# Kernel optimization log

Hardware: AMD Instinct MI355X
Metric: run time of the kernel (lower is better)

The kernel has to match this reference:

```python
import jax, jax.numpy as jnp
import numpy as np

EPS = 1e-6  # flax LayerNorm default

def _layer_norm(x, scale, bias):
    mu = jnp.mean(x, axis=-1, keepdims=True)
    var = jnp.mean(jnp.square(x - mu), axis=-1, keepdims=True)
    return (x - mu) * jax.lax.rsqrt(var + EPS) * scale + bias

def setup_inputs() -> dict:
    key = jax.random.key(0)
    ks = jax.random.split(key, 8)
    B, S, D_in, D_h, D_out, N = 4, 2048, 1024, 2048, 1024, 6
    init = lambda k, shape, fan_in: jax.random.normal(k, shape, jnp.float32) / np.sqrt(fan_in)
    return {
        "x": jax.random.normal(ks[0], (B, S, D_in), jnp.float32),
        "ln1_scale": jnp.ones((D_in,), jnp.float32),
        "ln1_bias": jnp.zeros((D_in,), jnp.float32),
        "w1": init(ks[1], (D_in, D_h), D_in),
        "b1": jnp.zeros((D_h,), jnp.float32),
        "block_ln_scales": jnp.ones((N, D_h), jnp.float32),
        "block_ln_biases": jnp.zeros((N, D_h), jnp.float32),
        "block_ws": init(ks[2], (N, D_h, D_h), D_h),
        "block_bs": jnp.zeros((N, D_h), jnp.float32),
        "ln2_scale": jnp.ones((D_h,), jnp.float32),
        "ln2_bias": jnp.zeros((D_h,), jnp.float32),
        "w2": init(ks[3], (D_h, D_out), D_h),
        "b2": jnp.zeros((D_out,), jnp.float32),
    }

def reference(x, ln1_scale, ln1_bias, w1, b1, block_ln_scales, block_ln_biases,
              block_ws, block_bs, ln2_scale, ln2_bias, w2, b2):
    # stem: LN -> Linear -> SiLU
    h = _layer_norm(x, ln1_scale, ln1_bias)
    h = jax.nn.silu(jnp.einsum('bsd,dh->bsh', h, w1) + b1)

    # residual blocks via scan over stacked params
    def block(h, params):
        s, b, w, lb = params
        y = _layer_norm(h, s, b)
        y = jax.nn.silu(jnp.einsum('bsh,hk->bsk', y, w) + lb)
        return h + y, None

    h, _ = jax.lax.scan(block, h, (block_ln_scales, block_ln_biases, block_ws, block_bs))

    # head: LN -> Linear
    h = _layer_norm(h, ln2_scale, ln2_bias)
    return jnp.einsum('bsh,ho->bso', h, w2) + b2
```

## Files before the change

kernel.cpp:

```cpp
#include <hip/hip_runtime.h>
#include <hip/hip_bf16.h>

typedef short short8 __attribute__((ext_vector_type(8)));
typedef float f32x4 __attribute__((ext_vector_type(4)));

#define AS1(p) ((const __attribute__((address_space(1))) void*)(p))
#define AS3(p) ((__attribute__((address_space(3))) void*)(p))

__device__ __forceinline__ ushort f2bf(float f) {
  __hip_bfloat16 h = __float2bfloat16(f);
  return *reinterpret_cast<const ushort*>(&h);
}
__device__ __forceinline__ float bfu2f(ushort u) {
  unsigned int x = ((unsigned int)u) << 16;
  float f;
  __builtin_memcpy(&f, &x, 4);
  return f;
}
__device__ __forceinline__ float silu_f(float v) { return v / (1.f + __expf(-v)); }

template<int NV>
__global__ __launch_bounds__(256) void ln_bf16_k(
    const float* __restrict__ in, const float* __restrict__ sc,
    const float* __restrict__ bi, ushort* __restrict__ out)
{
  const int D = NV * 1024;
  const long row = blockIdx.x;
  const int tx = threadIdx.x;
  const float* p = in + row * (long)D;
  float4 v[NV];
  float s = 0.f, s2 = 0.f;
#pragma unroll
  for (int t = 0; t < NV; ++t) {
    v[t] = *reinterpret_cast<const float4*>(p + t * 1024 + tx * 4);
    s  += v[t].x + v[t].y + v[t].z + v[t].w;
    s2 += v[t].x * v[t].x + v[t].y * v[t].y + v[t].z * v[t].z + v[t].w * v[t].w;
  }
#pragma unroll
  for (int o = 1; o < 64; o <<= 1) { s += __shfl_xor(s, o); s2 += __shfl_xor(s2, o); }
  __shared__ float red[2][4];
  const int wave = tx >> 6;
  if ((tx & 63) == 0) { red[0][wave] = s; red[1][wave] = s2; }
  __syncthreads();
  s  = red[0][0] + red[0][1] + red[0][2] + red[0][3];
  s2 = red[1][0] + red[1][1] + red[1][2] + red[1][3];
  const float mu   = s / D;
  const float rstd = rsqrtf(s2 / D - mu * mu + 1e-6f);
#pragma unroll
  for (int t = 0; t < NV; ++t) {
    const int d = t * 1024 + tx * 4;
    float4 g = *reinterpret_cast<const float4*>(sc + d);
    float4 b = *reinterpret_cast<const float4*>(bi + d);
    ushort4 o;
    o.x = f2bf((v[t].x - mu) * rstd * g.x + b.x);
    o.y = f2bf((v[t].y - mu) * rstd * g.y + b.y);
    o.z = f2bf((v[t].z - mu) * rstd * g.z + b.z);
    o.w = f2bf((v[t].w - mu) * rstd * g.w + b.w);
    *reinterpret_cast<ushort4*>(out + row * (long)D + d) = o;
  }
}

__global__ __launch_bounds__(256) void ln_stats_k(
    const ushort* __restrict__ in, float2* __restrict__ stats)
{
  const long row = blockIdx.x;
  const int tx = threadIdx.x;
  short8 v8 = *reinterpret_cast<const short8*>(in + row * 2048 + tx * 8);
  float s = 0.f, s2 = 0.f;
#pragma unroll
  for (int j = 0; j < 8; ++j) {
    const float v = bfu2f((ushort)v8[j]);
    s += v; s2 += v * v;
  }
#pragma unroll
  for (int o = 1; o < 64; o <<= 1) { s += __shfl_xor(s, o); s2 += __shfl_xor(s2, o); }
  __shared__ float red[2][4];
  const int wave = tx >> 6;
  if ((tx & 63) == 0) { red[0][wave] = s; red[1][wave] = s2; }
  __syncthreads();
  if (tx == 0) {
    s  = red[0][0] + red[0][1] + red[0][2] + red[0][3];
    s2 = red[1][0] + red[1][1] + red[1][2] + red[1][3];
    const float mu   = s * (1.f / 2048.f);
    const float rstd = rsqrtf(s2 * (1.f / 2048.f) - mu * mu + 1e-6f);
    stats[row] = make_float2(mu * rstd, rstd);
  }
}

__global__ __launch_bounds__(256) void transpose_bf16_k(
    const float* __restrict__ in, ushort* __restrict__ out, int K, int N)
{
  __shared__ float tile[64][65];
  const int k0 = blockIdx.y * 64, n0 = blockIdx.x * 64;
  const int tx = threadIdx.x, ty = threadIdx.y;
#pragma unroll
  for (int r = ty; r < 64; r += 4)
    tile[r][tx] = in[(long)(k0 + r) * N + n0 + tx];
  __syncthreads();
#pragma unroll
  for (int r = ty; r < 64; r += 4)
    out[(long)(n0 + r) * K + k0 + tx] = f2bf(tile[tx][r]);
}

__global__ __launch_bounds__(256) void transpose_scale_k(
    const float* __restrict__ in0, const float* __restrict__ g0,
    const float* __restrict__ beta0, ushort* __restrict__ out0,
    float2* __restrict__ uvw0, int K, int N)
{
  __shared__ float tile[64][65];
  const int z = blockIdx.z;
  const float* in    = in0 + (long)z * K * N;
  const float* g     = g0 + (long)z * K;
  const float* beta  = beta0 + (long)z * K;
  ushort* out        = out0 + (long)z * K * N;
  float2* uvw        = uvw0 + (long)z * N;
  const int k0 = blockIdx.y * 64, n0 = blockIdx.x * 64;
  const int tx = threadIdx.x, ty = threadIdx.y;
  float pu = 0.f, pv = 0.f;
#pragma unroll
  for (int r = ty; r < 64; r += 4) {
    const float w  = in[(long)(k0 + r) * N + n0 + tx];
    const float ws = g[k0 + r] * w;
    tile[r][tx] = ws;
    pu += ws;
    pv += beta[k0 + r] * w;
  }
  atomicAdd(&uvw[n0 + tx].x, pu);
  atomicAdd(&uvw[n0 + tx].y, pv);
  __syncthreads();
#pragma unroll
  for (int r = ty; r < 64; r += 4)
    out[(long)(n0 + r) * K + k0 + tx] = f2bf(tile[tx][r]);
}

__global__ __launch_bounds__(512) void combine_k(
    float* __restrict__ out, const float* __restrict__ part)
{
  const long i = ((long)blockIdx.x * 512 + threadIdx.x) * 4;
  float4 a = *reinterpret_cast<const float4*>(out + i);
  float4 b = *reinterpret_cast<const float4*>(part + i);
  a.x += b.x; a.y += b.y; a.z += b.z; a.w += b.w;
  *reinterpret_cast<float4*>(out + i) = a;
}

#define STG(gsrc, ldst)                                                          \
  __builtin_amdgcn_global_load_lds(AS1(gsrc),          AS3(ldst),          16, 0, 0); \
  __builtin_amdgcn_global_load_lds(AS1((gsrc) + offQ), AS3((ldst) + 8192), 16, 0, 0)

#define ldsA(B, H) (ldsW + (B) * 65536 + (H) * 16384)
#define ldsB(B, H) (ldsW + (B) * 65536 + 32768 + (H) * 16384)

#define RD_AF(DST, DB, MH, KS)                                                  \
  _Pragma("unroll") for (int i_ = 0; i_ < 4; ++i_)                              \
    DST[i_] = *(const short8*)(smem + (DB) * 65536 + aOff + ((MH) * 4 + i_) * 2048 + rdk[(KS)])

#define RD_BF(DST, DB, KS)                                                      \
  _Pragma("unroll") for (int j_ = 0; j_ < 4; ++j_)                              \
    DST[j_] = *(const short8*)(smem + (DB) * 65536 + bOff + j_ * 2048 + rdk[(KS)])

#define MFMA16(AREG, MH, BREG)                                                  \
  _Pragma("unroll") for (int i_ = 0; i_ < 4; ++i_)                              \
  _Pragma("unroll") for (int j_ = 0; j_ < 4; ++j_)                              \
    acc[(MH) * 4 + i_][j_] = __builtin_amdgcn_mfma_f32_16x16x32_bf16(           \
        AREG[i_], BREG[j_], acc[(MH) * 4 + i_][j_], 0, 0, 0)

#define BARRIER __builtin_amdgcn_s_barrier()
#define SP1 __builtin_amdgcn_s_setprio(1)
#define SP0 __builtin_amdgcn_s_setprio(0)
#define SBAR __builtin_amdgcn_sched_barrier(0)
#define LGKMW(N) do { asm volatile("s_waitcnt lgkmcnt(" #N ")"); SBAR; } while (0)
#define W4 do { asm volatile("s_waitcnt vmcnt(4)" ::: "memory"); SBAR; } while (0)
#define W0 do { asm volatile("s_waitcnt vmcnt(0)" ::: "memory"); SBAR; } while (0)
#define WN do {} while (0)

#define DO_TILE(DB, S1, AO, S2, BO, WAITE)                                      \
  RD_AF(afx, DB, 0, 0);                                                         \
  RD_BF(bf, DB, 0);                                                             \
  RD_AF(afy, DB, 1, 0);                                                         \
  if (S1) { STG(aP + (AO), ldsA((DB) ^ 1, 0));                                  \
            STG(aP + (AO) + offH, ldsA((DB) ^ 1, 1)); }                         \
  LGKMW(4);                                                                     \
  SP1; MFMA16(afx, 0, bf); SP0;                                                 \
  RD_AF(afx, DB, 0, 1);                                                         \
  LGKMW(4);                                                                     \
  SP1; MFMA16(afy, 1, bf); SP0;                                                 \
  RD_BF(bf, DB, 1);                                                             \
  SBAR;                                                                         \
  RD_AF(afy, DB, 1, 1);                                                         \
  LGKMW(4);                                                                     \
  SP1; MFMA16(afx, 0, bf); SP0;                                                 \
  BARRIER;                                                                      \
  if (S2) { STG(bP + (BO), ldsB(DB, 0));                                        \
            STG(bP + (BO) + offH, ldsB(DB, 1)); }                               \
  LGKMW(0);                                                                     \
  SP1; MFMA16(afy, 1, bf); SP0;                                                 \
  WAITE;                                                                        \
  BARRIER;

template<int MODE>
__global__ __launch_bounds__(512, 2) void gemm256_k(
    const ushort* __restrict__ A, const ushort* __restrict__ Bt,
    const float* __restrict__ bias, const float2* __restrict__ stats,
    const float2* __restrict__ uvw, const ushort* __restrict__ Rin,
    void* __restrict__ Cv, float* __restrict__ Cv2,
    int M, int N, int K, int ld)
{
  extern __shared__ char smem[];
  const int tid = threadIdx.x;
  const int lane = tid & 63, wid = tid >> 6;
  const int wr = wid >> 2, wc = wid & 3;
  const int nbx = N >> 8;

  int bid;
  {
    const int b = blockIdx.x;
    const int cpx = gridDim.x >> 3;
    bid = (b & 7) * cpx + (b >> 3);
  }
  int kb = 0;
  if (MODE == 5) { kb = bid >> 7; bid &= 127; }
  const int bx = bid % nbx, by = bid / nbx;
  const long m0 = (long)by << 8, n0 = (long)bx << 8;

  const int srow = tid >> 3;
  const int scol = (((tid & 7) * 16) ^ (((tid >> 3) & 7) << 4)) >> 1;
  const ushort* aP = A  + (long)kb * 1024 + (m0 + srow) * (long)ld + scol;
  const ushort* bP = Bt + (long)kb * 1024 + (n0 + srow) * (long)ld + scol;
  const long offH = 128L * ld, offQ = 64L * ld;
  char* ldsW = smem + wid * 1024;

  int rdk[2];
  rdk[0] = (((lane >> 4) * 16)     ) ^ ((lane & 7) << 4);
  rdk[1] = (((lane >> 4) * 16) + 64) ^ ((lane & 7) << 4);
  const int aOff = wr * 16384 + (lane & 15) * 128;
  const int bOff = 32768 + (wc >> 1) * 16384 + ((wc & 1) * 64 + (lane & 15)) * 128;

  f32x4 acc[8][4] = {};
  const int NT = K >> 6;

  STG(aP,      ldsA(0, 0));  STG(aP + offH,      ldsA(0, 1));
  STG(bP,      ldsB(0, 0));  STG(bP + offH,      ldsB(0, 1));
  STG(bP + 64, ldsB(1, 0));  STG(bP + 64 + offH, ldsB(1, 1));
  W4;
  BARRIER;

  short8 afx[4], afy[4], bf[4];
  for (int t = 0; t < NT - 2; t += 2) {
    DO_TILE(0, 1,  64, 1, 128, W4)
    DO_TILE(1, 1, 128, 1, 192, W4)
    aP += 128; bP += 128;
  }
  DO_TILE(0, 1, 64, 0, 0, W0)
  DO_TILE(1, 0,  0, 0, 0, WN)

  if (MODE == 0) {
#pragma unroll
    for (int j = 0; j < 4; ++j) {
      const long col = n0 + wc * 64 + j * 16 + (lane & 15);
      const float bj = bias[col];
#pragma unroll
      for (int i = 0; i < 8; ++i) {
        const long rowb = m0 + wr * 128 + i * 16 + ((lane >> 4) << 2);
#pragma unroll
        for (int r = 0; r < 4; ++r) {
          const float v = acc[i][j][r] + bj;
          ((ushort*)Cv)[(rowb + r) * N + col] = f2bf(silu_f(v));
        }
      }
    }
  } else {
    float2 uvv[4];
    float  bj4[4];
    long   col4[4];
#pragma unroll
    for (int j = 0; j < 4; ++j) {
      col4[j] = n0 + wc * 64 + j * 16 + (lane & 15);
      uvv[j]  = uvw[col4[j]];
      bj4[j]  = bias[col4[j]];
    }
    float* dst = (MODE == 5 && kb == 1) ? Cv2 : (float*)Cv;
    const float cw = (MODE == 5 && kb == 1) ? 0.f : 1.f;
#pragma unroll
    for (int i = 0; i < 8; ++i) {
      const long rowb = m0 + wr * 128 + i * 16 + ((lane >> 4) << 2);
#pragma unroll
      for (int r = 0; r < 4; ++r) {
        const long row = rowb + r;
        const float2 ms = stats[row];
#pragma unroll
        for (int j = 0; j < 4; ++j) {
          const long idx = row * (long)N + col4[j];
          if (MODE == 3) {
            const float v = ms.y * acc[i][j][r] - ms.x * uvv[j].x + uvv[j].y + bj4[j];
            ((ushort*)Cv)[idx] = f2bf(bfu2f(Rin[idx]) + silu_f(v));
          } else {
            const float v = ms.y * acc[i][j][r]
                          + cw * (uvv[j].y + bj4[j] - ms.x * uvv[j].x);
            dst[idx] = v;
          }
        }
      }
    }
  }
}

extern "C" void kernel_launch(void* const* d_in, const int* in_sizes, int n_in,
                              void* d_out, int out_size, void* d_ws, size_t ws_size,
                              hipStream_t stream) {
  const float* x     = (const float*)d_in[0];
  const float* ln1_s = (const float*)d_in[1];
  const float* ln1_b = (const float*)d_in[2];
  const float* w1    = (const float*)d_in[3];
  const float* b1    = (const float*)d_in[4];
  const float* bln_s = (const float*)d_in[5];
  const float* bln_b = (const float*)d_in[6];
  const float* bws   = (const float*)d_in[7];
  const float* bbs   = (const float*)d_in[8];
  const float* ln2_s = (const float*)d_in[9];
  const float* ln2_b = (const float*)d_in[10];
  const float* w2    = (const float*)d_in[11];
  const float* b2    = (const float*)d_in[12];
  float* out = (float*)d_out;

  const int M = 8192;
  char* ws = (char*)d_ws;
  ushort* h0    = (ushort*)ws;
  ushort* h1    = (ushort*)(ws + 33554432);
  ushort* Abf   = h1;
  ushort* wt    = (ushort*)(ws + 67108864);
  float2* uvw   = (float2*)(ws + 125829120);
  float2* stats = (float2*)(ws + 125829120 + 131072);
  const long W1T = 0;
  const long BLK = 2097152;
  const long W2T = BLK + 6L * 4194304;

  (void)hipFuncSetAttribute((const void*)gemm256_k<0>,
      hipFuncAttributeMaxDynamicSharedMemorySize, 131072);
  (void)hipFuncSetAttribute((const void*)gemm256_k<3>,
      hipFuncAttributeMaxDynamicSharedMemorySize, 131072);
  (void)hipFuncSetAttribute((const void*)gemm256_k<5>,
      hipFuncAttributeMaxDynamicSharedMemorySize, 131072);

  (void)hipMemsetAsync(uvw, 0, 7 * 2048 * sizeof(float2), stream);

  dim3 tb(64, 4);
  transpose_bf16_k<<<dim3(32, 16), tb, 0, stream>>>(w1, wt + W1T, 1024, 2048);
  transpose_scale_k<<<dim3(32, 32, 6), tb, 0, stream>>>(
      bws, bln_s, bln_b, wt + BLK, uvw, 2048, 2048);
  transpose_scale_k<<<dim3(16, 32, 1), tb, 0, stream>>>(
      w2, ln2_s, ln2_b, wt + W2T, uvw + 6L * 2048, 2048, 1024);

  ln_bf16_k<1><<<M, 256, 0, stream>>>(x, ln1_s, ln1_b, Abf);
  gemm256_k<0><<<32 * 8, 512, 131072, stream>>>(
      Abf, wt + W1T, b1, nullptr, nullptr, nullptr,
      (void*)h0, nullptr, M, 2048, 1024, 1024);

  ushort* hin = h0;
  ushort* hout = h1;
  for (int i = 0; i < 6; ++i) {
    ln_stats_k<<<M, 256, 0, stream>>>(hin, stats);
    gemm256_k<3><<<32 * 8, 512, 131072, stream>>>(
        hin, wt + BLK + (long)i * 4194304, bbs + i * 2048, stats,
        uvw + (long)i * 2048, hin, (void*)hout, nullptr, M, 2048, 2048, 2048);
    ushort* tmp = hin; hin = hout; hout = tmp;
  }

  float* part = (float*)h1;
  ln_stats_k<<<M, 256, 0, stream>>>(hin, stats);
  gemm256_k<5><<<32 * 4 * 2, 512, 131072, stream>>>(
      hin, wt + W2T, b2, stats, uvw + 6L * 2048, nullptr,
      (void*)out, part, M, 1024, 1024, 2048);
  combine_k<<<4096, 512, 0, stream>>>(out, part);
}
```

Before: 650.4 us.

## Fuse LayerNorm row statistics into GEMM epilogue with partial-sum reduction

Result: slower. 688.2 us (+5.8%).

```diff
diff --git a/kernel.cpp b/kernel.cpp
--- a/kernel.cpp
+++ b/kernel.cpp
@@ -60,33 +60,6 @@
   }
 }
 
-__global__ __launch_bounds__(256) void ln_stats_k(
-    const ushort* __restrict__ in, float2* __restrict__ stats)
-{
-  const long row = blockIdx.x;
-  const int tx = threadIdx.x;
-  short8 v8 = *reinterpret_cast<const short8*>(in + row * 2048 + tx * 8);
-  float s = 0.f, s2 = 0.f;
-#pragma unroll
-  for (int j = 0; j < 8; ++j) {
-    const float v = bfu2f((ushort)v8[j]);
-    s += v; s2 += v * v;
-  }
-#pragma unroll
-  for (int o = 1; o < 64; o <<= 1) { s += __shfl_xor(s, o); s2 += __shfl_xor(s2, o); }
-  __shared__ float red[2][4];
-  const int wave = tx >> 6;
-  if ((tx & 63) == 0) { red[0][wave] = s; red[1][wave] = s2; }
-  __syncthreads();
-  if (tx == 0) {
-    s  = red[0][0] + red[0][1] + red[0][2] + red[0][3];
-    s2 = red[1][0] + red[1][1] + red[1][2] + red[1][3];
-    const float mu   = s * (1.f / 2048.f);
-    const float rstd = rsqrtf(s2 * (1.f / 2048.f) - mu * mu + 1e-6f);
-    stats[row] = make_float2(mu * rstd, rstd);
-  }
-}
-
 __global__ __launch_bounds__(256) void transpose_bf16_k(
     const float* __restrict__ in, ushort* __restrict__ out, int K, int N)
 {
@@ -131,6 +104,22 @@
 #pragma unroll
   for (int r = ty; r < 64; r += 4)
     out[(long)(n0 + r) * K + k0 + tx] = f2bf(tile[tx][r]);
+}
+
+__global__ __launch_bounds__(256) void stats_reduce_k(
+    const float2* __restrict__ pstat, float2* __restrict__ stats)
+{
+  const int row = blockIdx.x * 256 + threadIdx.x;
+  const float4* p = reinterpret_cast<const float4*>(pstat + (long)row * 32);
+  float s = 0.f, s2 = 0.f;
+#pragma unroll
+  for (int q = 0; q < 16; ++q) {
+    const float4 v = p[q];
+    s += v.x + v.z; s2 += v.y + v.w;
+  }
+  const float mu   = s * (1.f / 2048.f);
+  const float rstd = rsqrtf(s2 * (1.f / 2048.f) - mu * mu + 1e-6f);
+  stats[row] = make_float2(mu * rstd, rstd);
 }
 
 __global__ __launch_bounds__(512) void combine_k(
@@ -202,7 +191,7 @@
     const ushort* __restrict__ A, const ushort* __restrict__ Bt,
     const float* __restrict__ bias, const float2* __restrict__ stats,
     const float2* __restrict__ uvw, const ushort* __restrict__ Rin,
-    void* __restrict__ Cv, float* __restrict__ Cv2,
+    float2* __restrict__ pstat, void* __restrict__ Cv, float* __restrict__ Cv2,
     int M, int N, int K, int ld)
 {
   extern __shared__ char smem[];
@@ -253,52 +242,50 @@
   DO_TILE(0, 1, 64, 0, 0, W0)
   DO_TILE(1, 0,  0, 0, 0, WN)
 
-  if (MODE == 0) {
-#pragma unroll
-    for (int j = 0; j < 4; ++j) {
-      const long col = n0 + wc * 64 + j * 16 + (lane & 15);
-      const float bj = bias[col];
-#pragma unroll
-      for (int i = 0; i < 8; ++i) {
-        const long rowb = m0 + wr * 128 + i * 16 + ((lane >> 4) << 2);
-#pragma unroll
-        for (int r = 0; r < 4; ++r) {
-          const float v = acc[i][j][r] + bj;
-          ((ushort*)Cv)[(rowb + r) * N + col] = f2bf(silu_f(v));
+  long  col4[4];
+  float bj4[4];
+  float2 uvv[4];
+#pragma unroll
+  for (int j = 0; j < 4; ++j) {
+    col4[j] = n0 + wc * 64 + j * 16 + (lane & 15);
+    bj4[j]  = bias[col4[j]];
+    if (MODE != 0) uvv[j] = uvw[col4[j]];
+  }
+  float* dst = (MODE == 5 && kb == 1) ? Cv2 : (float*)Cv;
+  const float cw = (MODE == 5 && kb == 1) ? 0.f : 1.f;
+#pragma unroll
+  for (int i = 0; i < 8; ++i) {
+#pragma unroll
+    for (int r = 0; r < 4; ++r) {
+      const long row = m0 + wr * 128 + i * 16 + ((lane >> 4) << 2) + r;
+      float2 ms = make_float2(0.f, 1.f);
+      if (MODE != 0) ms = stats[row];
+      float ps = 0.f, ps2 = 0.f;
+#pragma unroll
+      for (int j = 0; j < 4; ++j) {
+        const long idx = row * (long)N + col4[j];
+        if (MODE == 0) {
+          const float hv = silu_f(acc[i][j][r] + bj4[j]);
+          ((ushort*)Cv)[idx] = f2bf(hv);
+          ps += hv; ps2 += hv * hv;
+        } else if (MODE == 3) {
+          const float v = ms.y * acc[i][j][r] - ms.x * uvv[j].x + uvv[j].y + bj4[j];
+          const float hv = bfu2f(Rin[idx]) + silu_f(v);
+          ((ushort*)Cv)[idx] = f2bf(hv);
+          ps += hv; ps2 += hv * hv;
+        } else {
+          const float v = ms.y * acc[i][j][r]
+                        + cw * (uvv[j].y + bj4[j] - ms.x * uvv[j].x);
+          dst[idx] = v;
         }
       }
-    }
-  } else {
-    float2 uvv[4];
-    float  bj4[4];
-    long   col4[4];
-#pragma unroll
-    for (int j = 0; j < 4; ++j) {
-      col4[j] = n0 + wc * 64 + j * 16 + (lane & 15);
-      uvv[j]  = uvw[col4[j]];
-      bj4[j]  = bias[col4[j]];
-    }
-    float* dst = (MODE == 5 && kb == 1) ? Cv2 : (float*)Cv;
-    const float cw = (MODE == 5 && kb == 1) ? 0.f : 1.f;
-#pragma unroll
-    for (int i = 0; i < 8; ++i) {
-      const long rowb = m0 + wr * 128 + i * 16 + ((lane >> 4) << 2);
-#pragma unroll
-      for (int r = 0; r < 4; ++r) {
-        const long row = rowb + r;
-        const float2 ms = stats[row];
-#pragma unroll
-        for (int j = 0; j < 4; ++j) {
-          const long idx = row * (long)N + col4[j];
-          if (MODE == 3) {
-            const float v = ms.y * acc[i][j][r] - ms.x * uvv[j].x + uvv[j].y + bj4[j];
-            ((ushort*)Cv)[idx] = f2bf(bfu2f(Rin[idx]) + silu_f(v));
-          } else {
-            const float v = ms.y * acc[i][j][r]
-                          + cw * (uvv[j].y + bj4[j] - ms.x * uvv[j].x);
-            dst[idx] = v;
-          }
-        }
+      if (MODE == 0 || MODE == 3) {
+        ps  += __shfl_xor(ps, 1);  ps2 += __shfl_xor(ps2, 1);
+        ps  += __shfl_xor(ps, 2);  ps2 += __shfl_xor(ps2, 2);
+        ps  += __shfl_xor(ps, 4);  ps2 += __shfl_xor(ps2, 4);
+        ps  += __shfl_xor(ps, 8);  ps2 += __shfl_xor(ps2, 8);
+        if ((lane & 15) == 0)
+          pstat[row * 32 + bx * 4 + wc] = make_float2(ps, ps2);
       }
     }
   }
@@ -330,6 +317,7 @@
   ushort* wt    = (ushort*)(ws + 67108864);
   float2* uvw   = (float2*)(ws + 125829120);
   float2* stats = (float2*)(ws + 125829120 + 131072);
+  float2* pstat = (float2*)(ws + 125829120 + 131072 + 65536);
   const long W1T = 0;
   const long BLK = 2097152;
   const long W2T = BLK + 6L * 4194304;
@@ -352,23 +340,24 @@
 
   ln_bf16_k<1><<<M, 256, 0, stream>>>(x, ln1_s, ln1_b, Abf);
   gemm256_k<0><<<32 * 8, 512, 131072, stream>>>(
-      Abf, wt + W1T, b1, nullptr, nullptr, nullptr,
+      Abf, wt + W1T, b1, nullptr, nullptr, nullptr, pstat,
       (void*)h0, nullptr, M, 2048, 1024, 1024);
+  stats_reduce_k<<<32, 256, 0, stream>>>(pstat, stats);
 
   ushort* hin = h0;
   ushort* hout = h1;
   for (int i = 0; i < 6; ++i) {
-    ln_stats_k<<<M, 256, 0, stream>>>(hin, stats);
     gemm256_k<3><<<32 * 8, 512, 131072, stream>>>(
         hin, wt + BLK + (long)i * 4194304, bbs + i * 2048, stats,
-        uvw + (long)i * 2048, hin, (void*)hout, nullptr, M, 2048, 2048, 2048);
+        uvw + (long)i * 2048, hin, pstat, (void*)hout, nullptr,
+        M, 2048, 2048, 2048);
+    stats_reduce_k<<<32, 256, 0, stream>>>(pstat, stats);
     ushort* tmp = hin; hin = hout; hout = tmp;
   }
 
   float* part = (float*)h1;
-  ln_stats_k<<<M, 256, 0, stream>>>(hin, stats);
   gemm256_k<5><<<32 * 4 * 2, 512, 131072, stream>>>(
-      hin, wt + W2T, b2, stats, uvw + 6L * 2048, nullptr,
+      hin, wt + W2T, b2, stats, uvw + 6L * 2048, nullptr, nullptr,
       (void*)out, part, M, 1024, 1024, 2048);
   combine_k<<<4096, 512, 0, stream>>>(out, part);
 }
```

## Switch GEMM to 32x32x16 MFMA tiles and replace atomic uv sums with reduction

Applied to the files above, without the earlier changes.

Measured after the change: 699.7 us. +7.6%, slower.

```diff
diff --git a/kernel.cpp b/kernel.cpp
--- a/kernel.cpp
+++ b/kernel.cpp
@@ -2,7 +2,7 @@
 #include <hip/hip_bf16.h>
 
 typedef short short8 __attribute__((ext_vector_type(8)));
-typedef float f32x4 __attribute__((ext_vector_type(4)));
+typedef float f32x16 __attribute__((ext_vector_type(16)));
 
 #define AS1(p) ((const __attribute__((address_space(1))) void*)(p))
 #define AS3(p) ((__attribute__((address_space(3))) void*)(p))
@@ -105,15 +105,15 @@
 __global__ __launch_bounds__(256) void transpose_scale_k(
     const float* __restrict__ in0, const float* __restrict__ g0,
     const float* __restrict__ beta0, ushort* __restrict__ out0,
-    float2* __restrict__ uvw0, int K, int N)
+    float2* __restrict__ pup, int K, int N)
 {
   __shared__ float tile[64][65];
+  __shared__ float2 pred[4][64];
   const int z = blockIdx.z;
   const float* in    = in0 + (long)z * K * N;
   const float* g     = g0 + (long)z * K;
   const float* beta  = beta0 + (long)z * K;
   ushort* out        = out0 + (long)z * K * N;
-  float2* uvw        = uvw0 + (long)z * N;
   const int k0 = blockIdx.y * 64, n0 = blockIdx.x * 64;
   const int tx = threadIdx.x, ty = threadIdx.y;
   float pu = 0.f, pv = 0.f;
@@ -125,12 +125,29 @@
     pu += ws;
     pv += beta[k0 + r] * w;
   }
-  atomicAdd(&uvw[n0 + tx].x, pu);
-  atomicAdd(&uvw[n0 + tx].y, pv);
+  pred[ty][tx] = make_float2(pu, pv);
   __syncthreads();
+  if (ty == 0) {
+    const float2 a = pred[0][tx], b = pred[1][tx], c = pred[2][tx], d = pred[3][tx];
+    const long ZN = (long)gridDim.z * N;
+    pup[(long)blockIdx.y * ZN + (long)z * N + n0 + tx] =
+        make_float2(a.x + b.x + c.x + d.x, a.y + b.y + c.y + d.y);
+  }
 #pragma unroll
   for (int r = ty; r < 64; r += 4)
     out[(long)(n0 + r) * K + k0 + tx] = f2bf(tile[tx][r]);
+}
+
+__global__ __launch_bounds__(256) void uv_reduce_k(
+    const float2* __restrict__ pup, float2* __restrict__ uvw, int NK, int ZN)
+{
+  const int c = blockIdx.x * 256 + threadIdx.x;
+  float sx = 0.f, sy = 0.f;
+  for (int k = 0; k < NK; ++k) {
+    const float2 v = pup[(long)k * ZN + c];
+    sx += v.x; sy += v.y;
+  }
+  uvw[c] = make_float2(sx, sy);
 }
 
 __global__ __launch_bounds__(512) void combine_k(
@@ -150,19 +167,19 @@
 #define ldsA(B, H) (ldsW + (B) * 65536 + (H) * 16384)
 #define ldsB(B, H) (ldsW + (B) * 65536 + 32768 + (H) * 16384)
 
-#define RD_AF(DST, DB, MH, KS)                                                  \
+#define RD_A32(DST, DB, KS)                                                     \
   _Pragma("unroll") for (int i_ = 0; i_ < 4; ++i_)                              \
-    DST[i_] = *(const short8*)(smem + (DB) * 65536 + aOff + ((MH) * 4 + i_) * 2048 + rdk[(KS)])
-
-#define RD_BF(DST, DB, KS)                                                      \
-  _Pragma("unroll") for (int j_ = 0; j_ < 4; ++j_)                              \
-    DST[j_] = *(const short8*)(smem + (DB) * 65536 + bOff + j_ * 2048 + rdk[(KS)])
-
-#define MFMA16(AREG, MH, BREG)                                                  \
-  _Pragma("unroll") for (int i_ = 0; i_ < 4; ++i_)                              \
-  _Pragma("unroll") for (int j_ = 0; j_ < 4; ++j_)                              \
-    acc[(MH) * 4 + i_][j_] = __builtin_amdgcn_mfma_f32_16x16x32_bf16(           \
-        AREG[i_], BREG[j_], acc[(MH) * 4 + i_][j_], 0, 0, 0)
+    DST[i_] = *(const short8*)(smem + (DB) * 65536 + aB + i_ * 4096 + rdk32[(KS)])
+
+#define RD_B32(DST, DB, KS)                                                     \
+  _Pragma("unroll") for (int j_ = 0; j_ < 2; ++j_)                              \
+    DST[j_] = *(const short8*)(smem + (DB) * 65536 + bB + j_ * 4096 + rdk32[(KS)])
+
+#define MFMA8(AR, BR)                                                           \
+  _Pragma("unroll") for (int rt_ = 0; rt_ < 4; ++rt_)                           \
+  _Pragma("unroll") for (int ct_ = 0; ct_ < 2; ++ct_)                           \
+    acc[rt_][ct_] = __builtin_amdgcn_mfma_f32_32x32x16_bf16(                    \
+        AR[rt_], BR[ct_], acc[rt_][ct_], 0, 0, 0)
 
 #define BARRIER __builtin_amdgcn_s_barrier()
 #define SP1 __builtin_amdgcn_s_setprio(1)
@@ -173,27 +190,28 @@
 #define W0 do { asm volatile("s_waitcnt vmcnt(0)" ::: "memory"); SBAR; } while (0)
 #define WN do {} while (0)
 
-#define DO_TILE(DB, S1, AO, S2, BO, WAITE)                                      \
-  RD_AF(afx, DB, 0, 0);                                                         \
-  RD_BF(bf, DB, 0);                                                             \
-  RD_AF(afy, DB, 1, 0);                                                         \
+#define DO_TILE32(DB, S1, AO, S2, BO, WAITE)                                    \
+  RD_A32(ax, DB, 0);                                                            \
+  RD_B32(bx, DB, 0);                                                            \
   if (S1) { STG(aP + (AO), ldsA((DB) ^ 1, 0));                                  \
             STG(aP + (AO) + offH, ldsA((DB) ^ 1, 1)); }                         \
-  LGKMW(4);                                                                     \
-  SP1; MFMA16(afx, 0, bf); SP0;                                                 \
-  RD_AF(afx, DB, 0, 1);                                                         \
-  LGKMW(4);                                                                     \
-  SP1; MFMA16(afy, 1, bf); SP0;                                                 \
-  RD_BF(bf, DB, 1);                                                             \
-  SBAR;                                                                         \
-  RD_AF(afy, DB, 1, 1);                                                         \
-  LGKMW(4);                                                                     \
-  SP1; MFMA16(afx, 0, bf); SP0;                                                 \
+  RD_A32(ay, DB, 1);                                                            \
+  RD_B32(by, DB, 1);                                                            \
+  LGKMW(6);                                                                     \
+  SP1; MFMA8(ax, bx); SP0;                                                      \
+  RD_A32(ax, DB, 2);                                                            \
+  RD_B32(bx, DB, 2);                                                            \
+  LGKMW(6);                                                                     \
+  SP1; MFMA8(ay, by); SP0;                                                      \
+  RD_A32(ay, DB, 3);                                                            \
+  RD_B32(by, DB, 3);                                                            \
+  LGKMW(6);                                                                     \
+  SP1; MFMA8(ax, bx); SP0;                                                      \
   BARRIER;                                                                      \
   if (S2) { STG(bP + (BO), ldsB(DB, 0));                                        \
             STG(bP + (BO) + offH, ldsB(DB, 1)); }                               \
   LGKMW(0);                                                                     \
-  SP1; MFMA16(afy, 1, bf); SP0;                                                 \
+  SP1; MFMA8(ay, by); SP0;                                                      \
   WAITE;                                                                        \
   BARRIER;
 
@@ -229,13 +247,14 @@
   const long offH = 128L * ld, offQ = 64L * ld;
   char* ldsW = smem + wid * 1024;
 
-  int rdk[2];
-  rdk[0] = (((lane >> 4) * 16)     ) ^ ((lane & 7) << 4);
-  rdk[1] = (((lane >> 4) * 16) + 64) ^ ((lane & 7) << 4);
-  const int aOff = wr * 16384 + (lane & 15) * 128;
-  const int bOff = 32768 + (wc >> 1) * 16384 + ((wc & 1) * 64 + (lane & 15)) * 128;
-
-  f32x4 acc[8][4] = {};
+  int rdk32[4];
+#pragma unroll
+  for (int ks = 0; ks < 4; ++ks)
+    rdk32[ks] = (ks * 32 + ((lane >> 5) * 16)) ^ ((lane & 7) << 4);
+  const int aB = wr * 16384 + (lane & 31) * 128;
+  const int bB = 32768 + (wc >> 1) * 16384 + ((wc & 1) * 64 + (lane & 31)) * 128;
+
+  f32x16 acc[4][2] = {};
   const int NT = K >> 6;
 
   STG(aP,      ldsA(0, 0));  STG(aP + offH,      ldsA(0, 1));
@@ -244,60 +263,49 @@
   W4;
   BARRIER;
 
-  short8 afx[4], afy[4], bf[4];
+  short8 ax[4], ay[4], bx2[2], by2[2];
+#define bx bx2
+#define by by2
   for (int t = 0; t < NT - 2; t += 2) {
-    DO_TILE(0, 1,  64, 1, 128, W4)
-    DO_TILE(1, 1, 128, 1, 192, W4)
+    DO_TILE32(0, 1,  64, 1, 128, W4)
+    DO_TILE32(1, 1, 128, 1, 192, W4)
     aP += 128; bP += 128;
   }
-  DO_TILE(0, 1, 64, 0, 0, W0)
-  DO_TILE(1, 0,  0, 0, 0, WN)
-
-  if (MODE == 0) {
-#pragma unroll
-    for (int j = 0; j < 4; ++j) {
-      const long col = n0 + wc * 64 + j * 16 + (lane & 15);
-      const float bj = bias[col];
-#pragma unroll
-      for (int i = 0; i < 8; ++i) {
-        const long rowb = m0 + wr * 128 + i * 16 + ((lane >> 4) << 2);
-#pragma unroll
-        for (int r = 0; r < 4; ++r) {
-          const float v = acc[i][j][r] + bj;
-          ((ushort*)Cv)[(rowb + r) * N + col] = f2bf(silu_f(v));
-        }
-      }
-    }
-  } else {
-    float2 uvv[4];
-    float  bj4[4];
-    long   col4[4];
-#pragma unroll
-    for (int j = 0; j < 4; ++j) {
-      col4[j] = n0 + wc * 64 + j * 16 + (lane & 15);
-      uvv[j]  = uvw[col4[j]];
-      bj4[j]  = bias[col4[j]];
-    }
-    float* dst = (MODE == 5 && kb == 1) ? Cv2 : (float*)Cv;
-    const float cw = (MODE == 5 && kb == 1) ? 0.f : 1.f;
-#pragma unroll
-    for (int i = 0; i < 8; ++i) {
-      const long rowb = m0 + wr * 128 + i * 16 + ((lane >> 4) << 2);
-#pragma unroll
-      for (int r = 0; r < 4; ++r) {
-        const long row = rowb + r;
-        const float2 ms = stats[row];
-#pragma unroll
-        for (int j = 0; j < 4; ++j) {
-          const long idx = row * (long)N + col4[j];
-          if (MODE == 3) {
-            const float v = ms.y * acc[i][j][r] - ms.x * uvv[j].x + uvv[j].y + bj4[j];
-            ((ushort*)Cv)[idx] = f2bf(bfu2f(Rin[idx]) + silu_f(v));
-          } else {
-            const float v = ms.y * acc[i][j][r]
-                          + cw * (uvv[j].y + bj4[j] - ms.x * uvv[j].x);
-            dst[idx] = v;
-          }
+  DO_TILE32(0, 1, 64, 0, 0, W0)
+  DO_TILE32(1, 0,  0, 0, 0, WN)
+#undef bx
+#undef by
+
+  const int l5 = (lane >> 5) << 2;
+  long col2[2];
+  float bj2[2];
+  float2 uvv[2];
+#pragma unroll
+  for (int ct = 0; ct < 2; ++ct) {
+    col2[ct] = n0 + wc * 64 + ct * 32 + (lane & 31);
+    bj2[ct]  = bias[col2[ct]];
+    if (MODE != 0) uvv[ct] = uvw[col2[ct]];
+  }
+  float* dst = (MODE == 5 && kb == 1) ? Cv2 : (float*)Cv;
+  const float cw = (MODE == 5 && kb == 1) ? 0.f : 1.f;
+#pragma unroll
+  for (int rt = 0; rt < 4; ++rt) {
+#pragma unroll
+    for (int rg = 0; rg < 16; ++rg) {
+      const long row = m0 + wr * 128 + rt * 32 + (rg & 3) + 8 * (rg >> 2) + l5;
+      float2 ms = make_float2(0.f, 1.f);
+      if (MODE != 0) ms = stats[row];
+#pragma unroll
+      for (int ct = 0; ct < 2; ++ct) {
+        const long idx = row * (long)N + col2[ct];
+        if (MODE == 0) {
+          ((ushort*)Cv)[idx] = f2bf(silu_f(acc[rt][ct][rg] + bj2[ct]));
+        } else if (MODE == 3) {
+          const float v = ms.y * acc[rt][ct][rg] - ms.x * uvv[ct].x + uvv[ct].y + bj2[ct];
+          ((ushort*)Cv)[idx] = f2bf(bfu2f(Rin[idx]) + silu_f(v));
+        } else {
+          dst[idx] = ms.y * acc[rt][ct][rg]
+                   + cw * (uvv[ct].y + bj2[ct] - ms.x * uvv[ct].x);
         }
       }
     }
@@ -330,6 +338,8 @@
   ushort* wt    = (ushort*)(ws + 67108864);
   float2* uvw   = (float2*)(ws + 125829120);
   float2* stats = (float2*)(ws + 125829120 + 131072);
+  float2* pupA  = (float2*)(ws + 125829120 + 131072 + 65536);
+  float2* pupB  = (float2*)(ws + 125829120 + 131072 + 65536 + 3145728);
   const long W1T = 0;
   const long BLK = 2097152;
   const long W2T = BLK + 6L * 4194304;
@@ -341,14 +351,14 @@
   (void)hipFuncSetAttribute((const void*)gemm256_k<5>,
       hipFuncAttributeMaxDynamicSharedMemorySize, 131072);
 
-  (void)hipMemsetAsync(uvw, 0, 7 * 2048 * sizeof(float2), stream);
-
   dim3 tb(64, 4);
   transpose_bf16_k<<<dim3(32, 16), tb, 0, stream>>>(w1, wt + W1T, 1024, 2048);
   transpose_scale_k<<<dim3(32, 32, 6), tb, 0, stream>>>(
-      bws, bln_s, bln_b, wt + BLK, uvw, 2048, 2048);
+      bws, bln_s, bln_b, wt + BLK, pupA, 2048, 2048);
+  uv_reduce_k<<<48, 256, 0, stream>>>(pupA, uvw, 32, 12288);
   transpose_scale_k<<<dim3(16, 32, 1), tb, 0, stream>>>(
-      w2, ln2_s, ln2_b, wt + W2T, uvw + 6L * 2048, 2048, 1024);
+      w2, ln2_s, ln2_b, wt + W2T, pupB, 2048, 1024);
+  uv_reduce_k<<<4, 256, 0, stream>>>(pupB, uvw + 6L * 2048, 32, 1024);
 
   ln_bf16_k<1><<<M, 256, 0, stream>>>(x, ln1_s, ln1_b, Abf);
   gemm256_k<0><<<32 * 8, 512, 131072, stream>>>(
```
